# Kernel optimization log

Hardware: AMD Instinct MI355X
Metric: run time of the kernel (lower is better)

Reference implementation:

```python
import jax, jax.numpy as jnp
import numpy as np

D_MODEL = 256
N_HEADS = 4
D_FF = 1024
N = 6144
N_DOMS = 1024
LN_EPS = 1e-5
NEG_INF = -1e30


def setup_inputs() -> dict:
    key = jax.random.key(0)
    ks = jax.random.split(key, 10)
    x = jax.random.normal(ks[0], (N, D_MODEL), dtype=jnp.float32)
    pulse_to_dom_idx = jnp.sort(jax.random.randint(ks[1], (N,), 0, N_DOMS, dtype=jnp.int32))
    s = 0.02
    return {
        "x": x,
        "pulse_to_dom_idx": pulse_to_dom_idx,
        "qkv_w": jax.random.normal(ks[2], (D_MODEL, 3 * D_MODEL), dtype=jnp.float32) * s,
        "qkv_b": jnp.zeros((3 * D_MODEL,), dtype=jnp.float32),
        "out_w": jax.random.normal(ks[3], (D_MODEL, D_MODEL), dtype=jnp.float32) * s,
        "out_b": jnp.zeros((D_MODEL,), dtype=jnp.float32),
        "ff_w1": jax.random.normal(ks[4], (D_MODEL, D_FF), dtype=jnp.float32) * s,
        "ff_b1": jnp.zeros((D_FF,), dtype=jnp.float32),
        "ff_w2": jax.random.normal(ks[5], (D_FF, D_MODEL), dtype=jnp.float32) * s,
        "ff_b2": jnp.zeros((D_MODEL,), dtype=jnp.float32),
        "ln1_g": jnp.ones((D_MODEL,), dtype=jnp.float32),
        "ln1_b": jnp.zeros((D_MODEL,), dtype=jnp.float32),
        "ln2_g": jnp.ones((D_MODEL,), dtype=jnp.float32),
        "ln2_b": jnp.zeros((D_MODEL,), dtype=jnp.float32),
    }


def _layer_norm(x, g, b):
    mu = jnp.mean(x, axis=-1, keepdims=True)
    var = jnp.mean(jnp.square(x - mu), axis=-1, keepdims=True)
    return (x - mu) * jax.lax.rsqrt(var + LN_EPS) * g + b


def reference(x, pulse_to_dom_idx, qkv_w, qkv_b, out_w, out_b,
              ff_w1, ff_b1, ff_w2, ff_b2, ln1_g, ln1_b, ln2_g, ln2_b):
    n, d = x.shape
    hd = d // N_HEADS
    # --- document-masked multi-head attention (dense, matching FlexAttention score_mod) ---
    qkv = x @ qkv_w + qkv_b                      # (N, 3D)
    q, k, v = jnp.split(qkv, 3, axis=-1)
    q = q.reshape(n, N_HEADS, hd)
    k = k.reshape(n, N_HEADS, hd)
    v = v.reshape(n, N_HEADS, hd)
    scores = jnp.einsum('qhd,khd->hqk', q, k) / jnp.sqrt(jnp.float32(hd))  # (H, N, N)
    same_doc = pulse_to_dom_idx[:, None] == pulse_to_dom_idx[None, :]      # (N, N)
    scores = jnp.where(same_doc[None], scores, NEG_INF)
    attn = jax.nn.softmax(scores, axis=-1)
    attn_out = jnp.einsum('hqk,khd->qhd', attn, v).reshape(n, d)
    attn_out = attn_out @ out_w + out_b
    # --- residual + norm + FFN + residual + norm (dropout in eval mode) ---
    x = _layer_norm(x + attn_out, ln1_g, ln1_b)
    ff = jax.nn.gelu(x @ ff_w1 + ff_b1, approximate=False) @ ff_w2 + ff_b2
    x = _layer_norm(x + ff, ln2_g, ln2_b)
    return x
```

## Files before the change

### kernel.cpp

```cpp
#include <hip/hip_runtime.h>
#include <hip/hip_bf16.h>
#include <math.h>

constexpr int NP  = 6144;
constexpr int DM  = 256;
constexpr int DFF = 1024;
constexpr float LNEPS = 1e-5f;

typedef __attribute__((ext_vector_type(8))) short short8;
typedef __attribute__((ext_vector_type(4))) short short4v;
typedef __attribute__((ext_vector_type(4))) float f32x4;

__device__ __forceinline__ short f2bf(float f) {
    unsigned u = __builtin_bit_cast(unsigned, f);
    unsigned r = u + 0x7FFFu + ((u >> 16) & 1u);
    return (short)(r >> 16);
}
__device__ __forceinline__ float bf2f(short s) {
    unsigned u = ((unsigned)(unsigned short)s) << 16;
    return __builtin_bit_cast(float, u);
}

#define GLOAD16(gp, lp)                                                        \
    __builtin_amdgcn_global_load_lds(                                          \
        (const __attribute__((address_space(1))) unsigned int*)(gp),           \
        (__attribute__((address_space(3))) unsigned int*)(lp), 16, 0, 0)

__device__ __forceinline__ int lds_idx(int row, int chunk) {
    return row * 64 + ((chunk ^ (row & 7)) * 8);
}

__global__ __launch_bounds__(256) void prep_kernel(
    const float* __restrict__ qkv_w, const float* __restrict__ out_w,
    const float* __restrict__ ff_w1, const float* __restrict__ ff_w2,
    short* __restrict__ qkvT, short* __restrict__ outT,
    short* __restrict__ ff1T, short* __restrict__ ff2T,
    const int* __restrict__ dom, int* __restrict__ seg_s,
    int* __restrict__ seg_e, const float* __restrict__ x,
    short* __restrict__ xB) {
    int b = blockIdx.x;
    if (b >= 792) {
        int i = (b - 792) * 2048 + threadIdx.x * 8;
        float4 a0 = *(const float4*)&x[i];
        float4 a1 = *(const float4*)&x[i + 4];
        short8 v = { f2bf(a0.x), f2bf(a0.y), f2bf(a0.z), f2bf(a0.w),
                     f2bf(a1.x), f2bf(a1.y), f2bf(a1.z), f2bf(a1.w) };
        *(short8*)&xB[i] = v;
        return;
    }
    if (b >= 768) {
        int i = (b - 768) * 256 + threadIdx.x;
        if (i >= NP) return;
        int d = dom[i];
        int s = i;
        while (s > 0 && dom[s - 1] == d) --s;
        int e = i + 1;
        while (e < NP && dom[e] == d) ++e;
        seg_s[i] = s;
        seg_e[i] = e;
        return;
    }
    const float* src;
    short* dst;
    int K, Nn;
    if (b < 192)      { src = qkv_w; dst = qkvT; K = 256;  Nn = 768; }
    else if (b < 256) { b -= 192; src = out_w; dst = outT; K = 256;  Nn = 256; }
    else if (b < 512) { b -= 256; src = ff_w1; dst = ff1T; K = 256;  Nn = 1024; }
    else              { b -= 512; src = ff_w2; dst = ff2T; K = 1024; Nn = 256; }
    int tpr = Nn / 32;
    int k0 = (b / tpr) * 32, n0 = (b % tpr) * 32;

    __shared__ float lds[32][36];
    int t = threadIdx.x;
    {
        int k = t >> 3, n = (t & 7) * 4;
        *(float4*)&lds[k][n] = *(const float4*)&src[(size_t)(k0 + k) * Nn + n0 + n];
    }
    __syncthreads();
    {
        int n = t >> 3, ks = (t & 7) * 4;
        short4v o = { f2bf(lds[ks + 0][n]), f2bf(lds[ks + 1][n]),
                      f2bf(lds[ks + 2][n]), f2bf(lds[ks + 3][n]) };
        *(short4v*)&dst[(size_t)(n0 + n) * K + k0 + ks] = o;
    }
}

template <int EPI>
__global__ __launch_bounds__(256) void mgemm64(
    const short* __restrict__ A, const short* __restrict__ Bt,
    const float* __restrict__ bias, const short* __restrict__ res,
    void* __restrict__ Cv, int Nn, int K) {
    __shared__ __align__(16) short As[64 * 64];
    __shared__ __align__(16) short Bs[64 * 64];

    const int tid = threadIdx.x, lane = tid & 63, w = tid >> 6;
    const int wm = (w >> 1) * 32, wn = (w & 1) * 32;
    const int rowBase = blockIdx.y * 64, colBase = blockIdx.x * 64;
    const int lr = lane >> 3, sc = (lane & 7) ^ lr;
    const int fr = lane & 15, g4 = lane >> 4;

    f32x4 acc[2][2];
#pragma unroll
    for (int i = 0; i < 2; ++i)
#pragma unroll
        for (int j = 0; j < 2; ++j) acc[i][j] = f32x4{0.f, 0.f, 0.f, 0.f};

    for (int k0 = 0; k0 < K; k0 += 64) {
#pragma unroll
        for (int i = 0; i < 2; ++i) {
            int g = w * 2 + i;
            int row = g * 8 + lr;
            GLOAD16(A  + (size_t)(rowBase + row) * K + k0 + sc * 8, &As[g * 512]);
            GLOAD16(Bt + (size_t)(colBase + row) * K + k0 + sc * 8, &Bs[g * 512]);
        }
        __syncthreads();

#pragma unroll
        for (int kk = 0; kk < 2; ++kk) {
            int j = kk * 4 + g4;
            short8 af[2], bfv[2];
#pragma unroll
            for (int f = 0; f < 2; ++f) {
                af[f]  = *(const short8*)&As[lds_idx(wm + f * 16 + fr, j)];
                bfv[f] = *(const short8*)&Bs[lds_idx(wn + f * 16 + fr, j)];
            }
#pragma unroll
            for (int fm = 0; fm < 2; ++fm)
#pragma unroll
                for (int fn = 0; fn < 2; ++fn)
                    acc[fm][fn] = __builtin_amdgcn_mfma_f32_16x16x32_bf16(
                        af[fm], bfv[fn], acc[fm][fn], 0, 0, 0);
        }
        __syncthreads();
    }

    const int cr = g4 * 4;
#pragma unroll
    for (int fm = 0; fm < 2; ++fm)
#pragma unroll
        for (int fn = 0; fn < 2; ++fn) {
            int c = colBase + wn + fn * 16 + fr;
            float bv = bias[c];
#pragma unroll
            for (int j = 0; j < 4; ++j) {
                int r = rowBase + wm + fm * 16 + cr + j;
                float v = acc[fm][fn][j] + bv;
                if (EPI == 1) v = 0.5f * v * (1.0f + erff(v * 0.70710678118654752f));
                if (EPI == 2)
                    ((float*)Cv)[(size_t)r * Nn + c] =
                        v + bf2f(res[(size_t)r * 256 + c]);
                else
                    ((short*)Cv)[(size_t)r * Nn + c] = f2bf(v);
            }
        }
}

__global__ __launch_bounds__(256) void ln_kernel(
    const float* __restrict__ in, const float* __restrict__ g,
    const float* __restrict__ b, float* __restrict__ out) {
    int wid = blockIdx.x * 4 + (threadIdx.x >> 6);
    int lane = threadIdx.x & 63;

    float4 v = ((const float4*)(in + (size_t)wid * 256))[lane];
    float s = v.x + v.y + v.z + v.w;
#pragma unroll
    for (int off = 32; off; off >>= 1) s += __shfl_xor(s, off);
    float mu = s * (1.0f / 256.0f);
    float dx = v.x - mu, dy = v.y - mu, dz = v.z - mu, dw = v.w - mu;
    float ss = dx * dx + dy * dy + dz * dz + dw * dw;
#pragma unroll
    for (int off = 32; off; off >>= 1) ss += __shfl_xor(ss, off);
    float rstd = rsqrtf(ss * (1.0f / 256.0f) + LNEPS);

    float4 gg = ((const float4*)g)[lane];
    float4 bb = ((const float4*)b)[lane];
    float4 o;
    o.x = dx * rstd * gg.x + bb.x;
    o.y = dy * rstd * gg.y + bb.y;
    o.z = dz * rstd * gg.z + bb.z;
    o.w = dw * rstd * gg.w + bb.w;
    ((float4*)(out + (size_t)wid * 256))[lane] = o;
}

__global__ __launch_bounds__(512) void attnln_kernel(
    const short* __restrict__ qkvB, const int* __restrict__ seg_s,
    const int* __restrict__ seg_e, const short* __restrict__ outT,
    const float* __restrict__ out_b, const float* __restrict__ xres,
    const float* __restrict__ gw, const float* __restrict__ bw,
    short* __restrict__ x1) {
    __shared__ __align__(16) short As[32 * 256];
    __shared__ __align__(16) short Bs[256 * 64];
    __shared__ float r1[8][32], r2[8][32];

    const int tid = threadIdx.x, lane = tid & 63, w = tid >> 6;
    const int rowBase = blockIdx.x * 32;
    const int lr = lane >> 3, sc = (lane & 7) ^ lr;
    const int fr = lane & 15, g4 = lane >> 4;

    {
        const int l8 = lane & 7;
        const int G  = (w << 3) | (lane >> 3);
#pragma unroll
        for (int s = 0; s < 2; ++s) {
            int task = G + s * 64;
            int r = task >> 2, h = task & 3;
            int row = rowBase + r;
            short8 qv = *(const short8*)&qkvB[(size_t)row * 768 + h * 64 + l8 * 8];
            float qd[8];
#pragma unroll
            for (int e = 0; e < 8; ++e) qd[e] = bf2f(qv[e]);
            int ss = seg_s[row], ee = seg_e[row];
            float m = -INFINITY, l = 0.0f;
            float acc[8] = {0.f, 0.f, 0.f, 0.f, 0.f, 0.f, 0.f, 0.f};
            for (int j = ss; j < ee; ++j) {
                short8 kv = *(const short8*)&qkvB[(size_t)j * 768 + 256 + h * 64 + l8 * 8];
                short8 vv = *(const short8*)&qkvB[(size_t)j * 768 + 512 + h * 64 + l8 * 8];
                float prod = 0.f;
#pragma unroll
                for (int e = 0; e < 8; ++e) prod += qd[e] * bf2f(kv[e]);
                prod += __shfl_xor(prod, 1);
                prod += __shfl_xor(prod, 2);
                prod += __shfl_xor(prod, 4);
                float score = prod * 0.125f;
                float mn = fmaxf(m, score);
                float scale = __expf(m - mn);
                float p = __expf(score - mn);
                l = l * scale + p;
#pragma unroll
                for (int e = 0; e < 8; ++e) acc[e] = acc[e] * scale + p * bf2f(vv[e]);
                m = mn;
            }
            float inv = 1.0f / l;
            int c = h * 8 + l8;
            short8 o;
#pragma unroll
            for (int e = 0; e < 8; ++e) o[e] = f2bf(acc[e] * inv);
            *(short8*)&As[r * 256 + ((c ^ (r & 7)) * 8)] = o;
        }
    }
    __syncthreads();

    f32x4 acc[2][2];
#pragma unroll
    for (int i = 0; i < 2; ++i)
#pragma unroll
        for (int j = 0; j < 2; ++j) acc[i][j] = f32x4{0.f, 0.f, 0.f, 0.f};

    for (int k0 = 0; k0 < 256; k0 += 64) {
#pragma unroll
        for (int i = 0; i < 4; ++i) {
            int g = w * 4 + i;
            GLOAD16(outT + (size_t)(g * 8 + lr) * 256 + k0 + sc * 8, &Bs[g * 512]);
        }
        __syncthreads();
#pragma unroll
        for (int kk = 0; kk < 2; ++kk) {
            int j = kk * 4 + g4;
            int cj = (k0 >> 3) + j;
            short8 af[2], bfv[2];
            af[0] = *(const short8*)&As[fr * 256 + ((cj ^ (fr & 7)) * 8)];
            af[1] = *(const short8*)&As[(16 + fr) * 256 + ((cj ^ (fr & 7)) * 8)];
#pragma unroll
            for (int fn = 0; fn < 2; ++fn)
                bfv[fn] = *(const short8*)&Bs[lds_idx(w * 32 + fn * 16 + fr, j)];
#pragma unroll
            for (int fm = 0; fm < 2; ++fm)
#pragma unroll
                for (int fn = 0; fn < 2; ++fn)
                    acc[fm][fn] = __builtin_amdgcn_mfma_f32_16x16x32_bf16(
                        af[fm], bfv[fn], acc[fm][fn], 0, 0, 0);
        }
        __syncthreads();
    }

    float v[2][2][4], p1[2][4], p2[2][4];
#pragma unroll
    for (int fm = 0; fm < 2; ++fm)
#pragma unroll
        for (int j = 0; j < 4; ++j) { p1[fm][j] = 0.f; p2[fm][j] = 0.f; }
#pragma unroll
    for (int fm = 0; fm < 2; ++fm)
#pragma unroll
        for (int fn = 0; fn < 2; ++fn) {
            int c = w * 32 + fn * 16 + fr;
            float bv = out_b[c];
#pragma unroll
            for (int j = 0; j < 4; ++j) {
                int r = rowBase + fm * 16 + g4 * 4 + j;
                float t = acc[fm][fn][j] + bv + xres[(size_t)r * 256 + c];
                v[fm][fn][j] = t;
                p1[fm][j] += t;
                p2[fm][j] += t * t;
            }
        }
#pragma unroll
    for (int m = 1; m < 16; m <<= 1)
#pragma unroll
        for (int fm = 0; fm < 2; ++fm)
#pragma unroll
            for (int j = 0; j < 4; ++j) {
                p1[fm][j] += __shfl_xor(p1[fm][j], m);
                p2[fm][j] += __shfl_xor(p2[fm][j], m);
            }
    if (fr == 0) {
#pragma unroll
        for (int fm = 0; fm < 2; ++fm)
#pragma unroll
            for (int j = 0; j < 4; ++j) {
                r1[w][fm * 16 + g4 * 4 + j] = p1[fm][j];
                r2[w][fm * 16 + g4 * 4 + j] = p2[fm][j];
            }
    }
    __syncthreads();
#pragma unroll
    for (int fm = 0; fm < 2; ++fm)
#pragma unroll
        for (int j = 0; j < 4; ++j) {
            int rl = fm * 16 + g4 * 4 + j;
            int r = rowBase + rl;
            float s1 = 0.f, s2 = 0.f;
#pragma unroll
            for (int ww = 0; ww < 8; ++ww) { s1 += r1[ww][rl]; s2 += r2[ww][rl]; }
            float mu = s1 * (1.0f / 256.0f);
            float var = s2 * (1.0f / 256.0f) - mu * mu;
            float rstd = rsqrtf(var + LNEPS);
#pragma unroll
            for (int fn = 0; fn < 2; ++fn) {
                int c = w * 32 + fn * 16 + fr;
                float o = (v[fm][fn][j] - mu) * rstd * gw[c] + bw[c];
                x1[(size_t)r * 256 + c] = f2bf(o);
            }
        }
}

extern "C" void kernel_launch(void* const* d_in, const int* in_sizes, int n_in,
                              void* d_out, int out_size, void* d_ws, size_t ws_size,
                              hipStream_t stream) {
    const float* x      = (const float*)d_in[0];
    const int*   dom    = (const int*)d_in[1];
    const float* qkv_w  = (const float*)d_in[2];
    const float* qkv_b  = (const float*)d_in[3];
    const float* out_w  = (const float*)d_in[4];
    const float* out_b  = (const float*)d_in[5];
    const float* ff_w1  = (const float*)d_in[6];
    const float* ff_b1  = (const float*)d_in[7];
    const float* ff_w2  = (const float*)d_in[8];
    const float* ff_b2  = (const float*)d_in[9];
    const float* ln1_g  = (const float*)d_in[10];
    const float* ln1_b  = (const float*)d_in[11];
    const float* ln2_g  = (const float*)d_in[12];
    const float* ln2_b  = (const float*)d_in[13];
    float* out = (float*)d_out;

    short* xB     = (short*)d_ws;
    short* qkvB   = xB + (size_t)NP * 256;
    short* x1     = qkvB + (size_t)NP * 768;
    short* hB     = x1 + (size_t)NP * 256;
    short* qkvT   = hB + (size_t)NP * 1024;
    short* outT   = qkvT + 768 * 256;
    short* ff1T   = outT + 256 * 256;
    short* ff2T   = ff1T + 1024 * 256;
    int* seg_s    = (int*)(ff2T + 256 * 1024);
    int* seg_e    = seg_s + NP;
    float* y      = (float*)(seg_e + NP);

    prep_kernel<<<1560, 256, 0, stream>>>(qkv_w, out_w, ff_w1, ff_w2,
                                          qkvT, outT, ff1T, ff2T,
                                          dom, seg_s, seg_e, x, xB);

    mgemm64<0><<<dim3(768 / 64, NP / 64), 256, 0, stream>>>(
        xB, qkvT, qkv_b, nullptr, qkvB, 768, 256);

    attnln_kernel<<<NP / 32, 512, 0, stream>>>(
        qkvB, seg_s, seg_e, outT, out_b, x, ln1_g, ln1_b, x1);

    mgemm64<1><<<dim3(DFF / 64, NP / 64), 256, 0, stream>>>(
        x1, ff1T, ff_b1, nullptr, hB, 1024, 256);

    mgemm64<2><<<dim3(DM / 64, NP / 64), 256, 0, stream>>>(
        hB, ff2T, ff_b2, x1, y, 256, 1024);

    ln_kernel<<<NP / 4, 256, 0, stream>>>(y, ln2_g, ln2_b, out);
}
```

Baseline: 68.22 us.

## Deepen GEMM K-tile, swizzle block order, halve attention rows per block

The generic GEMM now stages a 128-wide K slice per iteration, which halves the number of barrier and load rounds, and it remaps block IDs in an XCD-style interleave to improve cache locality. The fused attention+LN kernel now processes 16 rows per block instead of 32. That doubles the grid to spread the serial per-row softmax loop across more CUs, at the cost of reloading the out-projection weights twice as often. The larger LDS footprint in the GEMM may reduce occupancy.

New measurement: 60.03 us. 1.14x faster.

```diff
diff --git a/kernel.cpp b/kernel.cpp
--- a/kernel.cpp
+++ b/kernel.cpp
@@ -28,6 +28,9 @@
 
 __device__ __forceinline__ int lds_idx(int row, int chunk) {
     return row * 64 + ((chunk ^ (row & 7)) * 8);
+}
+__device__ __forceinline__ int lds_idx128(int row, int chunk) {
+    return row * 128 + ((chunk ^ (row & 7)) * 8);
 }
 
 __global__ __launch_bounds__(256) void prep_kernel(
@@ -90,13 +93,20 @@
     const short* __restrict__ A, const short* __restrict__ Bt,
     const float* __restrict__ bias, const short* __restrict__ res,
     void* __restrict__ Cv, int Nn, int K) {
-    __shared__ __align__(16) short As[64 * 64];
-    __shared__ __align__(16) short Bs[64 * 64];
+    __shared__ __align__(16) short As[64 * 128];
+    __shared__ __align__(16) short Bs[64 * 128];
 
     const int tid = threadIdx.x, lane = tid & 63, w = tid >> 6;
     const int wm = (w >> 1) * 32, wn = (w & 1) * 32;
-    const int rowBase = blockIdx.y * 64, colBase = blockIdx.x * 64;
-    const int lr = lane >> 3, sc = (lane & 7) ^ lr;
+
+    const int nx = gridDim.x;
+    const int bid = blockIdx.y * nx + blockIdx.x;
+    const int q = (nx * gridDim.y) >> 3;
+    const int id2 = (bid & 7) * q + (bid >> 3);
+    const int rowBase = (id2 / nx) * 64, colBase = (id2 % nx) * 64;
+
+    const int lr4 = lane >> 4;
+    const int c16 = lane & 15;
     const int fr = lane & 15, g4 = lane >> 4;
 
     f32x4 acc[2][2];
@@ -105,24 +115,25 @@
 #pragma unroll
         for (int j = 0; j < 2; ++j) acc[i][j] = f32x4{0.f, 0.f, 0.f, 0.f};
 
-    for (int k0 = 0; k0 < K; k0 += 64) {
-#pragma unroll
-        for (int i = 0; i < 2; ++i) {
-            int g = w * 2 + i;
-            int row = g * 8 + lr;
+    for (int k0 = 0; k0 < K; k0 += 128) {
+#pragma unroll
+        for (int i = 0; i < 4; ++i) {
+            int g = w * 4 + i;
+            int row = g * 4 + lr4;
+            int sc = c16 ^ (row & 7);
             GLOAD16(A  + (size_t)(rowBase + row) * K + k0 + sc * 8, &As[g * 512]);
             GLOAD16(Bt + (size_t)(colBase + row) * K + k0 + sc * 8, &Bs[g * 512]);
         }
         __syncthreads();
 
 #pragma unroll
-        for (int kk = 0; kk < 2; ++kk) {
+        for (int kk = 0; kk < 4; ++kk) {
             int j = kk * 4 + g4;
             short8 af[2], bfv[2];
 #pragma unroll
             for (int f = 0; f < 2; ++f) {
-                af[f]  = *(const short8*)&As[lds_idx(wm + f * 16 + fr, j)];
-                bfv[f] = *(const short8*)&Bs[lds_idx(wn + f * 16 + fr, j)];
+                af[f]  = *(const short8*)&As[lds_idx128(wm + f * 16 + fr, j)];
+                bfv[f] = *(const short8*)&Bs[lds_idx128(wn + f * 16 + fr, j)];
             }
 #pragma unroll
             for (int fm = 0; fm < 2; ++fm)
@@ -188,63 +199,57 @@
     const float* __restrict__ out_b, const float* __restrict__ xres,
     const float* __restrict__ gw, const float* __restrict__ bw,
     short* __restrict__ x1) {
-    __shared__ __align__(16) short As[32 * 256];
+    __shared__ __align__(16) short As[16 * 256];
     __shared__ __align__(16) short Bs[256 * 64];
-    __shared__ float r1[8][32], r2[8][32];
+    __shared__ float r1[8][16], r2[8][16];
 
     const int tid = threadIdx.x, lane = tid & 63, w = tid >> 6;
-    const int rowBase = blockIdx.x * 32;
+    const int rowBase = blockIdx.x * 16;
     const int lr = lane >> 3, sc = (lane & 7) ^ lr;
     const int fr = lane & 15, g4 = lane >> 4;
 
     {
         const int l8 = lane & 7;
         const int G  = (w << 3) | (lane >> 3);
-#pragma unroll
-        for (int s = 0; s < 2; ++s) {
-            int task = G + s * 64;
-            int r = task >> 2, h = task & 3;
-            int row = rowBase + r;
-            short8 qv = *(const short8*)&qkvB[(size_t)row * 768 + h * 64 + l8 * 8];
-            float qd[8];
-#pragma unroll
-            for (int e = 0; e < 8; ++e) qd[e] = bf2f(qv[e]);
-            int ss = seg_s[row], ee = seg_e[row];
-            float m = -INFINITY, l = 0.0f;
-            float acc[8] = {0.f, 0.f, 0.f, 0.f, 0.f, 0.f, 0.f, 0.f};
-            for (int j = ss; j < ee; ++j) {
-                short8 kv = *(const short8*)&qkvB[(size_t)j * 768 + 256 + h * 64 + l8 * 8];
-                short8 vv = *(const short8*)&qkvB[(size_t)j * 768 + 512 + h * 64 + l8 * 8];
-                float prod = 0.f;
-#pragma unroll
-                for (int e = 0; e < 8; ++e) prod += qd[e] * bf2f(kv[e]);
-                prod += __shfl_xor(prod, 1);
-                prod += __shfl_xor(prod, 2);
-                prod += __shfl_xor(prod, 4);
-                float score = prod * 0.125f;
-                float mn = fmaxf(m, score);
-                float scale = __expf(m - mn);
-                float p = __expf(score - mn);
-                l = l * scale + p;
-#pragma unroll
-                for (int e = 0; e < 8; ++e) acc[e] = acc[e] * scale + p * bf2f(vv[e]);
-                m = mn;
-            }
-            float inv = 1.0f / l;
-            int c = h * 8 + l8;
-            short8 o;
-#pragma unroll
-            for (int e = 0; e < 8; ++e) o[e] = f2bf(acc[e] * inv);
-            *(short8*)&As[r * 256 + ((c ^ (r & 7)) * 8)] = o;
-        }
+        int r = G >> 2, h = G & 3;
+        int row = rowBase + r;
+        short8 qv = *(const short8*)&qkvB[(size_t)row * 768 + h * 64 + l8 * 8];
+        float qd[8];
+#pragma unroll
+        for (int e = 0; e < 8; ++e) qd[e] = bf2f(qv[e]);
+        int ss = seg_s[row], ee = seg_e[row];
+        float m = -INFINITY, l = 0.0f;
+        float acc[8] = {0.f, 0.f, 0.f, 0.f, 0.f, 0.f, 0.f, 0.f};
+        for (int j = ss; j < ee; ++j) {
+            short8 kv = *(const short8*)&qkvB[(size_t)j * 768 + 256 + h * 64 + l8 * 8];
+            short8 vv = *(const short8*)&qkvB[(size_t)j * 768 + 512 + h * 64 + l8 * 8];
+            float prod = 0.f;
+#pragma unroll
+            for (int e = 0; e < 8; ++e) prod += qd[e] * bf2f(kv[e]);
+            prod += __shfl_xor(prod, 1);
+            prod += __shfl_xor(prod, 2);
+            prod += __shfl_xor(prod, 4);
+            float score = prod * 0.125f;
+            float mn = fmaxf(m, score);
+            float scale = __expf(m - mn);
+            float p = __expf(score - mn);
+            l = l * scale + p;
+#pragma unroll
+            for (int e = 0; e < 8; ++e) acc[e] = acc[e] * scale + p * bf2f(vv[e]);
+            m = mn;
+        }
+        float inv = 1.0f / l;
+        int c = h * 8 + l8;
+        short8 o;
+#pragma unroll
+        for (int e = 0; e < 8; ++e) o[e] = f2bf(acc[e] * inv);
+        *(short8*)&As[r * 256 + ((c ^ (r & 7)) * 8)] = o;
     }
     __syncthreads();
 
-    f32x4 acc[2][2];
-#pragma unroll
-    for (int i = 0; i < 2; ++i)
-#pragma unroll
-        for (int j = 0; j < 2; ++j) acc[i][j] = f32x4{0.f, 0.f, 0.f, 0.f};
+    f32x4 acc[2];
+    acc[0] = f32x4{0.f, 0.f, 0.f, 0.f};
+    acc[1] = f32x4{0.f, 0.f, 0.f, 0.f};
 
     for (int k0 = 0; k0 < 256; k0 += 64) {
 #pragma unroll
@@ -257,80 +262,67 @@
         for (int kk = 0; kk < 2; ++kk) {
             int j = kk * 4 + g4;
             int cj = (k0 >> 3) + j;
-            short8 af[2], bfv[2];
-            af[0] = *(const short8*)&As[fr * 256 + ((cj ^ (fr & 7)) * 8)];
-            af[1] = *(const short8*)&As[(16 + fr) * 256 + ((cj ^ (fr & 7)) * 8)];
+            short8 af = *(const short8*)&As[fr * 256 + ((cj ^ (fr & 7)) * 8)];
+            short8 bfv[2];
 #pragma unroll
             for (int fn = 0; fn < 2; ++fn)
                 bfv[fn] = *(const short8*)&Bs[lds_idx(w * 32 + fn * 16 + fr, j)];
 #pragma unroll
-            for (int fm = 0; fm < 2; ++fm)
-#pragma unroll
-                for (int fn = 0; fn < 2; ++fn)
-                    acc[fm][fn] = __builtin_amdgcn_mfma_f32_16x16x32_bf16(
-                        af[fm], bfv[fn], acc[fm][fn], 0, 0, 0);
+            for (int fn = 0; fn < 2; ++fn)
+                acc[fn] = __builtin_amdgcn_mfma_f32_16x16x32_bf16(
+                    af, bfv[fn], acc[fn], 0, 0, 0);
         }
         __syncthreads();
     }
 
-    float v[2][2][4], p1[2][4], p2[2][4];
-#pragma unroll
-    for (int fm = 0; fm < 2; ++fm)
-#pragma unroll
-        for (int j = 0; j < 4; ++j) { p1[fm][j] = 0.f; p2[fm][j] = 0.f; }
-#pragma unroll
-    for (int fm = 0; fm < 2; ++fm)
+    float v[2][4], p1[4], p2[4];
+#pragma unroll
+    for (int j = 0; j < 4; ++j) { p1[j] = 0.f; p2[j] = 0.f; }
+#pragma unroll
+    for (int fn = 0; fn < 2; ++fn) {
+        int c = w * 32 + fn * 16 + fr;
+        float bv = out_b[c];
+#pragma unroll
+        for (int j = 0; j < 4; ++j) {
+            int r = rowBase + g4 * 4 + j;
+            float t = acc[fn][j] + bv + xres[(size_t)r * 256 + c];
+            v[fn][j] = t;
+            p1[j] += t;
+            p2[j] += t * t;
+        }
+    }
+#pragma unroll
+    for (int m = 1; m < 16; m <<= 1)
+#pragma unroll
+        for (int j = 0; j < 4; ++j) {
+            p1[j] += __shfl_xor(p1[j], m);
+            p2[j] += __shfl_xor(p2[j], m);
+        }
+    if (fr == 0) {
+#pragma unroll
+        for (int j = 0; j < 4; ++j) {
+            r1[w][g4 * 4 + j] = p1[j];
+            r2[w][g4 * 4 + j] = p2[j];
+        }
+    }
+    __syncthreads();
+#pragma unroll
+    for (int j = 0; j < 4; ++j) {
+        int rl = g4 * 4 + j;
+        int r = rowBase + rl;
+        float s1 = 0.f, s2 = 0.f;
+#pragma unroll
+        for (int ww = 0; ww < 8; ++ww) { s1 += r1[ww][rl]; s2 += r2[ww][rl]; }
+        float mu = s1 * (1.0f / 256.0f);
+        float var = s2 * (1.0f / 256.0f) - mu * mu;
+        float rstd = rsqrtf(var + LNEPS);
 #pragma unroll
         for (int fn = 0; fn < 2; ++fn) {
             int c = w * 32 + fn * 16 + fr;
-            float bv = out_b[c];
-#pragma unroll
-            for (int j = 0; j < 4; ++j) {
-                int r = rowBase + fm * 16 + g4 * 4 + j;
-                float t = acc[fm][fn][j] + bv + xres[(size_t)r * 256 + c];
-                v[fm][fn][j] = t;
-                p1[fm][j] += t;
-                p2[fm][j] += t * t;
-            }
-        }
-#pragma unroll
-    for (int m = 1; m < 16; m <<= 1)
-#pragma unroll
-        for (int fm = 0; fm < 2; ++fm)
-#pragma unroll
-            for (int j = 0; j < 4; ++j) {
-                p1[fm][j] += __shfl_xor(p1[fm][j], m);
-                p2[fm][j] += __shfl_xor(p2[fm][j], m);
-            }
-    if (fr == 0) {
-#pragma unroll
-        for (int fm = 0; fm < 2; ++fm)
-#pragma unroll
-            for (int j = 0; j < 4; ++j) {
-                r1[w][fm * 16 + g4 * 4 + j] = p1[fm][j];
-                r2[w][fm * 16 + g4 * 4 + j] = p2[fm][j];
-            }
-    }
-    __syncthreads();
-#pragma unroll
-    for (int fm = 0; fm < 2; ++fm)
-#pragma unroll
-        for (int j = 0; j < 4; ++j) {
-            int rl = fm * 16 + g4 * 4 + j;
-            int r = rowBase + rl;
-            float s1 = 0.f, s2 = 0.f;
-#pragma unroll
-            for (int ww = 0; ww < 8; ++ww) { s1 += r1[ww][rl]; s2 += r2[ww][rl]; }
-            float mu = s1 * (1.0f / 256.0f);
-            float var = s2 * (1.0f / 256.0f) - mu * mu;
-            float rstd = rsqrtf(var + LNEPS);
-#pragma unroll
-            for (int fn = 0; fn < 2; ++fn) {
-                int c = w * 32 + fn * 16 + fr;
-                float o = (v[fm][fn][j] - mu) * rstd * gw[c] + bw[c];
-                x1[(size_t)r * 256 + c] = f2bf(o);
-            }
-        }
+            float o = (v[fn][j] - mu) * rstd * gw[c] + bw[c];
+            x1[(size_t)r * 256 + c] = f2bf(o);
+        }
+    }
 }
 
 extern "C" void kernel_launch(void* const* d_in, const int* in_sizes, int n_in,
@@ -371,7 +363,7 @@
     mgemm64<0><<<dim3(768 / 64, NP / 64), 256, 0, stream>>>(
         xB, qkvT, qkv_b, nullptr, qkvB, 768, 256);
 
-    attnln_kernel<<<NP / 32, 512, 0, stream>>>(
+    attnln_kernel<<<NP / 16, 512, 0, stream>>>(
         qkvB, seg_s, seg_e, outT, out_b, x, ln1_g, ln1_b, x1);
 
     mgemm64<1><<<dim3(DFF / 64, NP / 64), 256, 0, stream>>>(
```
